# Optimization experiments

Measured on AMD Instinct MI355X. Metric: run time of the kernel, lower is better.

## Reference

```python
import jax, jax.numpy as jnp
import numpy as np

ALPHA = 0.6       # blend weight alpha
SEM_W = 0.5       # semantic_weight
PATCH = 3         # patch_size
EPS = 1e-5


def _mean_std(feat):
    # torch .var(dim=2) uses the unbiased estimator (ddof=1)
    N, C = feat.shape[:2]
    f = feat.reshape(N, C, -1)
    var = jnp.var(f, axis=2, ddof=1) + EPS
    return f.mean(axis=2).reshape(N, C, 1, 1), jnp.sqrt(var).reshape(N, C, 1, 1)


def _project(feat):
    m, s = _mean_std(feat)
    return (feat - m) / s


def _unfold(x, p):
    # torch x.unfold(2,p,1).unfold(3,p,1).permute(0,2,3,1,4,5).reshape(-1,C,p,p)
    N, C, H, W = x.shape
    Ho, Wo = H - p + 1, W - p + 1
    pats = jnp.stack([x[:, :, i:i + Ho, j:j + Wo]
                      for i in range(p) for j in range(p)], axis=-1)  # [N,C,Ho,Wo,p*p]
    return pats.transpose(0, 2, 3, 1, 4).reshape(N * Ho * Wo, C, p, p)


def _sgtw(sF, sF_fused, cF_fused, p):
    style_patches = _unfold(sF, p)        # [K, C, p, p]
    fused_patches = _unfold(sF_fused, p)  # [K, Cf, p, p]
    K = fused_patches.shape[0]
    norm = jnp.sqrt(jnp.sum(fused_patches.reshape(K, -1) ** 2, axis=1)).reshape(K, 1, 1, 1)
    kernels = fused_patches / (norm + 1e-7)
    # cross-correlation: content fused features vs normalized style patches
    coord = jax.lax.conv_general_dilated(
        cF_fused, kernels, (1, 1), 'VALID',
        dimension_numbers=('NCHW', 'OIHW', 'NCHW'))  # [N, K, Ho, Wo]
    idx = jnp.argmax(coord, axis=1)       # [N, Ho, Wo] hard top-1 patch match
    # one-hot scatter + conv_transpose2d == gather best patch + overlap-add
    sel = style_patches[idx]              # [N, Ho, Wo, C, p, p]
    N, Ho, Wo = idx.shape
    C = style_patches.shape[1]
    Hout, Wout = Ho + p - 1, Wo + p - 1
    out = jnp.zeros((N, C, Hout, Wout), sel.dtype)
    cnt = jnp.zeros((Hout, Wout), sel.dtype)
    for i in range(p):
        for j in range(p):
            out = out.at[:, :, i:i + Ho, j:j + Wo].add(sel[:, :, :, :, i, j].transpose(0, 3, 1, 2))
            cnt = cnt.at[i:i + Ho, j:j + Wo].add(1.0)
    return out / cnt[None, None]  # overlap-normalized reconstruction


def setup_inputs() -> dict:
    key = jax.random.key(0)
    k1, k2, k3, k4 = jax.random.split(key, 4)
    N, C, Cs, H, W = 1, 512, 64, 64, 64
    return {
        'cF': jax.random.normal(k1, (N, C, H, W), jnp.float32),
        'sF': jax.random.normal(k2, (N, C, H, W), jnp.float32),
        'cF_sem': jax.random.normal(k3, (N, Cs, H, W), jnp.float32),
        'sF_sem': jax.random.normal(k4, (N, Cs, H, W), jnp.float32),
    }


def reference(cF, sF, cF_sem, sF_sem):
    # VSTR_concat
    sF1 = _project(sF)
    cF1 = _project(cF)
    sF_fused = jnp.concatenate([sF1, SEM_W * sF_sem], axis=1)
    cF_fused = jnp.concatenate([cF1, SEM_W * cF_sem], axis=1)
    target = _sgtw(sF, sF_fused, cF_fused, PATCH).reshape(cF.shape)
    return ALPHA * target + (1.0 - ALPHA) * cF
```

## Files before the change

### kernel.cpp

```cpp
#include <hip/hip_runtime.h>
#include <hip/hip_bf16.h>

#define HW      4096
#define WIDTH   64
#define C_MAIN  512
#define C_F     576
#define HO      62
#define KPATCH  3844
#define ALPHA_W 0.6f
#define SEM_W   0.5f
#define EPS_V   1e-5f
#define DELTA   4e-3f

typedef __attribute__((ext_vector_type(8))) short bf16x8;
typedef __attribute__((ext_vector_type(4))) float f32x4;

__global__ __launch_bounds__(256) void stats_kernel(
    const float* __restrict__ cF, const float* __restrict__ sF,
    float4* __restrict__ stats) {
  int b = blockIdx.x;
  int tensor = b >> 9, c = b & 511;
  const float* src = (tensor ? sF : cF) + (size_t)c * HW;
  int t = threadIdx.x;
  float sum = 0.f, sumsq = 0.f;
#pragma unroll
  for (int i = 0; i < 4; ++i) {
    float4 v = *(const float4*)(src + (i * 256 + t) * 4);
    sum   += v.x + v.y + v.z + v.w;
    sumsq += v.x * v.x + v.y * v.y + v.z * v.z + v.w * v.w;
  }
#pragma unroll
  for (int off = 32; off; off >>= 1) {
    sum   += __shfl_down(sum, off, 64);
    sumsq += __shfl_down(sumsq, off, 64);
  }
  __shared__ float ls[8];
  int lane = t & 63, wv = t >> 6;
  if (lane == 0) { ls[wv] = sum; ls[4 + wv] = sumsq; }
  __syncthreads();
  if (t == 0) {
    float s  = ls[0] + ls[1] + ls[2] + ls[3];
    float sq = ls[4] + ls[5] + ls[6] + ls[7];
    float mean = s / 4096.f;
    float var  = (sq - 4096.f * mean * mean) / 4095.f;
    float sig  = sqrtf(var + EPS_V);
    stats[b] = make_float4(mean, 1.f / sig, sig, 0.f);
  }
}

__global__ __launch_bounds__(256) void transform_kernel(
    const float* __restrict__ cF, const float* __restrict__ sF,
    const float* __restrict__ cSem, const float* __restrict__ sSem,
    const float4* __restrict__ stats,
    unsigned short* __restrict__ Ahi, unsigned short* __restrict__ Alo,
    unsigned short* __restrict__ Bhi, unsigned short* __restrict__ Blo,
    float* __restrict__ sFfT) {
  int tensor = blockIdx.z;
  int p0 = blockIdx.x * 32, k0 = blockIdx.y * 32;
  __shared__ float tile[32][33];
  int tx = threadIdx.x & 31, ty = threadIdx.x >> 5;
  for (int r = ty; r < 32; r += 8) {
    int ch = k0 + r;
    float x;
    if (ch < C_MAIN) {
      const float* src = tensor ? sF : cF;
      float4 st = stats[tensor * 512 + ch];
      x = (src[(size_t)ch * HW + p0 + tx] - st.x) * st.y;
    } else {
      const float* src = tensor ? sSem : cSem;
      x = SEM_W * src[(size_t)(ch - C_MAIN) * HW + p0 + tx];
    }
    tile[r][tx] = x;
  }
  __syncthreads();
  unsigned short* dhi = tensor ? Bhi : Ahi;
  unsigned short* dlo = tensor ? Blo : Alo;
  for (int r = ty; r < 32; r += 8) {
    float x = tile[tx][r];
    __hip_bfloat16 hb = __float2bfloat16(x);
    float hf = __bfloat162float(hb);
    __hip_bfloat16 lb = __float2bfloat16(x - hf);
    size_t o = (size_t)(p0 + r) * C_F + k0 + tx;
    dhi[o] = *reinterpret_cast<const unsigned short*>(&hb);
    dlo[o] = *reinterpret_cast<const unsigned short*>(&lb);
    if (tensor) sFfT[o] = x;
  }
}

__global__ __launch_bounds__(256) void gemm_kernel(
    const unsigned short* __restrict__ Ahi, const unsigned short* __restrict__ Alo,
    const unsigned short* __restrict__ Bhi, const unsigned short* __restrict__ Blo,
    float* __restrict__ M) {
  __shared__ __align__(16) unsigned short As_hi[128 * 32];
  __shared__ __align__(16) unsigned short As_lo[128 * 32];
  __shared__ __align__(16) unsigned short Bs_hi[128 * 32];
  __shared__ __align__(16) unsigned short Bs_lo[128 * 32];
  int a0 = blockIdx.x * 128, u0 = blockIdx.y * 128;
  int t = threadIdx.x;
  int lane = t & 63, wave = t >> 6;
  int wr = wave >> 1, wc = wave & 1;
  int l15 = lane & 15, hig = lane >> 4;

  int sr = t >> 2;
  int sc = (t & 3) * 8;
  const unsigned short* Ag0 = Ahi + (size_t)(a0 + sr) * C_F + sc;
  const unsigned short* Ag1 = Alo + (size_t)(a0 + sr) * C_F + sc;
  const unsigned short* Bg0 = Bhi + (size_t)(u0 + sr) * C_F + sc;
  const unsigned short* Bg1 = Blo + (size_t)(u0 + sr) * C_F + sc;
  const size_t rstep = (size_t)64 * C_F;

  uint4 pah0 = *(const uint4*)(Ag0), pah1 = *(const uint4*)(Ag0 + rstep);
  uint4 pal0 = *(const uint4*)(Ag1), pal1 = *(const uint4*)(Ag1 + rstep);
  uint4 pbh0 = *(const uint4*)(Bg0), pbh1 = *(const uint4*)(Bg0 + rstep);
  uint4 pbl0 = *(const uint4*)(Bg1), pbl1 = *(const uint4*)(Bg1 + rstep);

  f32x4 zero4 = {0.f, 0.f, 0.f, 0.f};
  f32x4 acc[4][4];
#pragma unroll
  for (int m = 0; m < 4; ++m)
#pragma unroll
    for (int n = 0; n < 4; ++n) acc[m][n] = zero4;

  int lw = sr * 4 + (t & 3);
  for (int k0 = 0; k0 < C_F; k0 += 32) {
    __syncthreads();
    ((uint4*)As_hi)[lw] = pah0; ((uint4*)As_hi)[lw + 256] = pah1;
    ((uint4*)As_lo)[lw] = pal0; ((uint4*)As_lo)[lw + 256] = pal1;
    ((uint4*)Bs_hi)[lw] = pbh0; ((uint4*)Bs_hi)[lw + 256] = pbh1;
    ((uint4*)Bs_lo)[lw] = pbl0; ((uint4*)Bs_lo)[lw + 256] = pbl1;
    __syncthreads();
    if (k0 + 32 < C_F) {
      Ag0 += 32; Ag1 += 32; Bg0 += 32; Bg1 += 32;
      pah0 = *(const uint4*)(Ag0); pah1 = *(const uint4*)(Ag0 + rstep);
      pal0 = *(const uint4*)(Ag1); pal1 = *(const uint4*)(Ag1 + rstep);
      pbh0 = *(const uint4*)(Bg0); pbh1 = *(const uint4*)(Bg0 + rstep);
      pbl0 = *(const uint4*)(Bg1); pbl1 = *(const uint4*)(Bg1 + rstep);
    }
    bf16x8 bh[4], bl[4];
#pragma unroll
    for (int n = 0; n < 4; ++n) {
      int brow = wc * 64 + n * 16 + l15;
      bh[n] = *(const bf16x8*)&Bs_hi[brow * 32 + hig * 8];
      bl[n] = *(const bf16x8*)&Bs_lo[brow * 32 + hig * 8];
    }
#pragma unroll
    for (int m = 0; m < 4; ++m) {
      int arow = wr * 64 + m * 16 + l15;
      bf16x8 ah = *(const bf16x8*)&As_hi[arow * 32 + hig * 8];
      bf16x8 al = *(const bf16x8*)&As_lo[arow * 32 + hig * 8];
#pragma unroll
      for (int n = 0; n < 4; ++n) {
        acc[m][n] = __builtin_amdgcn_mfma_f32_16x16x32_bf16(ah, bh[n], acc[m][n], 0, 0, 0);
        acc[m][n] = __builtin_amdgcn_mfma_f32_16x16x32_bf16(ah, bl[n], acc[m][n], 0, 0, 0);
        acc[m][n] = __builtin_amdgcn_mfma_f32_16x16x32_bf16(al, bh[n], acc[m][n], 0, 0, 0);
      }
    }
  }
#pragma unroll
  for (int m = 0; m < 4; ++m) {
    int row = a0 + wr * 64 + m * 16 + hig * 4;
#pragma unroll
    for (int n = 0; n < 4; ++n) {
      int col = u0 + wc * 64 + n * 16 + l15;
#pragma unroll
      for (int r = 0; r < 4; ++r)
        M[(size_t)(row + r) * HW + col] = acc[m][n][r];
    }
  }
}

__global__ __launch_bounds__(256) void colsumsq_kernel(
    const float* __restrict__ sFfT, float* __restrict__ q) {
  int row = blockIdx.x * 4 + (threadIdx.x >> 6);
  int lane = threadIdx.x & 63;
  const float* r = sFfT + (size_t)row * C_F;
  float s = 0.f;
  for (int i = lane; i < C_F; i += 64) { float v = r[i]; s += v * v; }
#pragma unroll
  for (int off = 32; off; off >>= 1) s += __shfl_down(s, off, 64);
  if (lane == 0) q[row] = s;
}

__global__ __launch_bounds__(256) void rnorm_kernel(
    const float* __restrict__ q, float* __restrict__ rnorm) {
  int k = blockIdx.x * 256 + threadIdx.x;
  if (k >= KPATCH) return;
  int ky = k / HO, kx = k - ky * HO;
  float s = 0.f;
#pragma unroll
  for (int i = 0; i < 3; ++i)
#pragma unroll
    for (int j = 0; j < 3; ++j) s += q[(ky + i) * WIDTH + kx + j];
  rnorm[k] = 1.f / (sqrtf(s) + 1e-7f);
}

__global__ __launch_bounds__(256) void argmax_kernel(
    const float* __restrict__ M, const float* __restrict__ rnorm,
    const float* __restrict__ sFfT,
    const float* __restrict__ cF, const float* __restrict__ cSem,
    const float4* __restrict__ stats,
    int* __restrict__ idx) {
  int y0 = blockIdx.x * 2;
  int x0 = min((int)blockIdx.y * 4, HO - 4);
  int t = threadIdx.x;

  const float* Mbase = M + (size_t)(y0 * WIDTH + x0) * HW;
  int ijo[9];
#pragma unroll
  for (int i = 0; i < 3; ++i)
#pragma unroll
    for (int j = 0; j < 3; ++j)
      ijo[i * 3 + j] = (i * WIDTH + j) * HW + i * WIDTH + j;

  float v1[8], v2[8];
  int   k1[8], k2[8];
#pragma unroll
  for (int p = 0; p < 8; ++p) { v1[p] = -1e30f; v2[p] = -1e30f; k1[p] = 0; k2[p] = 0; }

  for (int k = t; k < KPATCH; k += 256) {
    int ky = k / HO;
    int u = k + 2 * ky;
    float s[8];
#pragma unroll
    for (int p = 0; p < 8; ++p) s[p] = 0.f;
#pragma unroll
    for (int o = 0; o < 9; ++o) {
      const float* p9 = Mbase + ijo[o] + u;
#pragma unroll
      for (int py = 0; py < 2; ++py)
#pragma unroll
        for (int px = 0; px < 4; ++px)
          s[py * 4 + px] += p9[(size_t)(py * WIDTH + px) * HW];
    }
    float rn = rnorm[k];
#pragma unroll
    for (int p = 0; p < 8; ++p) {
      float v = s[p] * rn;
      if (v > v1[p]) { v2[p] = v1[p]; k2[p] = k1[p]; v1[p] = v; k1[p] = k; }
      else if (v > v2[p]) { v2[p] = v; k2[p] = k; }
    }
  }

  __shared__ float sv[256];
  __shared__ int   sk[256];
  __shared__ float redf[256];
  __shared__ float cpatch[9 * C_F];
  __shared__ int   candList[64];
  __shared__ int   candN;
  __shared__ float bestE;
  __shared__ int   bestK;

  for (int pp = 0; pp < 8; ++pp) {
    int py = pp >> 2, px = pp & 3;
    float mv1 = -1e30f, mv2 = -1e30f; int mk1 = 0;
#pragma unroll
    for (int q = 0; q < 8; ++q)
      if (q == pp) { mv1 = v1[q]; mv2 = v2[q]; mk1 = k1[q]; }

    __syncthreads();
    sv[t] = mv1; sk[t] = mk1;
    __syncthreads();
    for (int off = 128; off; off >>= 1) {
      if (t < off) {
        float ov = sv[t + off]; int ok = sk[t + off];
        if (ov > sv[t] || (ov == sv[t] && ok < sk[t])) { sv[t] = ov; sk[t] = ok; }
      }
      __syncthreads();
    }
    float vbest = sv[0];
    int   kbest = sk[0];
    float thr = vbest - DELTA;
    if (t == 0) candN = 0;
    __syncthreads();

    int poff = (py * WIDTH + px) * HW;
    if (mv2 >= thr) {
      for (int k = t; k < KPATCH; k += 256) {
        int ky = k / HO;
        int u = k + 2 * ky;
        float s = 0.f;
#pragma unroll
        for (int o = 0; o < 9; ++o) s += Mbase[(size_t)(poff + ijo[o]) + u];
        float v = s * rnorm[k];
        if (v >= thr && k != kbest) {
          int sl = atomicAdd(&candN, 1);
          if (sl < 64) candList[sl] = k;
        }
      }
    } else if (mv1 >= thr && mk1 != kbest) {
      int sl = atomicAdd(&candN, 1);
      if (sl < 64) candList[sl] = mk1;
    }
    __syncthreads();
    int nc = min(candN, 64);
    if (nc == 0) {
      if (t == 0) idx[(y0 + py) * HO + x0 + px] = kbest;
      continue;
    }

    int y = y0 + py, x = x0 + px;
    for (int f = t; f < 9 * C_F; f += 256) {
      int ij = f / C_F, c = f - ij * C_F;
      int pp2 = (y + ij / 3) * WIDTH + x + ij % 3;
      float cv;
      if (c < C_MAIN) {
        float4 st = stats[c];
        cv = (cF[(size_t)c * HW + pp2] - st.x) * st.y;
      } else {
        cv = SEM_W * cSem[(size_t)(c - C_MAIN) * HW + pp2];
      }
      cpatch[f] = cv;
    }
    __syncthreads();
    if (t == 0) { bestE = -1e30f; bestK = 0x7fffffff; }
    __syncthreads();

    for (int ci = -1; ci < nc; ++ci) {
      int k = (ci < 0) ? kbest : candList[ci];
      int ky = k / HO, kx = k - ky * HO;
      float part = 0.f;
      for (int f = t; f < 9 * C_F; f += 256) {
        int ij = f / C_F, c = f - ij * C_F;
        int sp = (ky + ij / 3) * WIDTH + kx + ij % 3;
        part += cpatch[f] * sFfT[(size_t)sp * C_F + c];
      }
      redf[t] = part;
      __syncthreads();
      for (int off = 128; off; off >>= 1) {
        if (t < off) redf[t] += redf[t + off];
        __syncthreads();
      }
      if (t == 0) {
        float e = redf[0] * rnorm[k];
        if (e > bestE || (e == bestE && k < bestK)) { bestE = e; bestK = k; }
      }
      __syncthreads();
    }
    if (t == 0) idx[(y0 + py) * HO + x0 + px] = bestK;
  }
}

__global__ __launch_bounds__(256) void gather_kernel(
    const float* __restrict__ sFfT, const int* __restrict__ idx,
    float* __restrict__ tmp) {
  __shared__ int srcs[9];
  __shared__ int nv;
  int pix = blockIdx.x;
  int h = pix >> 6, w = pix & 63;
  if (threadIdx.x == 0) {
    int n = 0;
    for (int i = 0; i < 3; ++i)
      for (int j = 0; j < 3; ++j) {
        int y = h - i, x = w - j;
        if (y >= 0 && y < HO && x >= 0 && x < HO) {
          int k = idx[y * HO + x];
          int ky = k / HO, kx = k - ky * HO;
          srcs[n++] = (ky + i) * WIDTH + kx + j;
        }
      }
    nv = n;
  }
  __syncthreads();
  int n = nv;
  for (int c = threadIdx.x; c < C_MAIN; c += 256) {
    float acc = 0.f;
    for (int s = 0; s < n; ++s) acc += sFfT[(size_t)srcs[s] * C_F + c];
    tmp[(size_t)pix * C_MAIN + c] = acc;
  }
}

__global__ void blend_kernel(
    const float* __restrict__ tmp, const float* __restrict__ cF,
    const float4* __restrict__ stats, float* __restrict__ out) {
  __shared__ float tile[32][33];
  int p0 = blockIdx.x * 32;
  int c0 = blockIdx.y * 32;
  int tx = threadIdx.x, ty = threadIdx.y;
  for (int r = ty; r < 32; r += 8)
    tile[r][tx] = tmp[(size_t)(p0 + r) * C_MAIN + c0 + tx];
  __syncthreads();
  for (int r = ty; r < 32; r += 8) {
    int pix = p0 + tx;
    int h = pix >> 6, w = pix & 63;
    int nh = min(2, h) - max(0, h - 61) + 1;
    int nw = min(2, w) - max(0, w - 61) + 1;
    float inv_cnt = 1.f / (float)(nh * nw);
    int c = c0 + r;
    float4 st = stats[512 + c];
    float recon = st.z * (tile[tx][r] * inv_cnt) + st.x;
    out[(size_t)c * HW + pix] =
        ALPHA_W * recon + (1.f - ALPHA_W) * cF[(size_t)c * HW + pix];
  }
}

extern "C" void kernel_launch(void* const* d_in, const int* in_sizes, int n_in,
                              void* d_out, int out_size, void* d_ws, size_t ws_size,
                              hipStream_t stream) {
  const float* cF   = (const float*)d_in[0];
  const float* sF   = (const float*)d_in[1];
  const float* cSem = (const float*)d_in[2];
  const float* sSem = (const float*)d_in[3];
  float* out = (float*)d_out;

  char* ws = (char*)d_ws;
  unsigned short* Ahi = (unsigned short*)ws;
  unsigned short* Alo = Ahi + (size_t)HW * C_F;
  unsigned short* Bhi = Alo + (size_t)HW * C_F;
  unsigned short* Blo = Bhi + (size_t)HW * C_F;
  float* tmp  = (float*)ws;
  float* M    = (float*)(ws + 18874368);
  float* sFfT = (float*)(ws + 85983232);
  float* q    = (float*)(ws + 95420416);
  float* rnrm = (float*)(ws + 95420416 + 16384);
  int*   idx  = (int*)  (ws + 95420416 + 32768);
  float4* stats = (float4*)(ws + 95420416 + 49152);

  stats_kernel<<<1024, 256, 0, stream>>>(cF, sF, stats);
  transform_kernel<<<dim3(HW / 32, C_F / 32, 2), 256, 0, stream>>>(
      cF, sF, cSem, sSem, stats, Ahi, Alo, Bhi, Blo, sFfT);
  colsumsq_kernel<<<HW / 4, 256, 0, stream>>>(sFfT, q);
  rnorm_kernel<<<(KPATCH + 255) / 256, 256, 0, stream>>>(q, rnrm);
  gemm_kernel<<<dim3(32, 32), 256, 0, stream>>>(Ahi, Alo, Bhi, Blo, M);
  argmax_kernel<<<dim3(31, 16), 256, 0, stream>>>(M, rnrm, sFfT, cF, cSem, stats, idx);
  gather_kernel<<<HW, 256, 0, stream>>>(sFfT, idx, tmp);
  blend_kernel<<<dim3(128, 16), dim3(32, 8), 0, stream>>>(tmp, cF, stats, out);
}
```

Baseline: 225.0 us.

## Split argmax over patch chunks into partial top-2 kernel plus merge kernel

The argmax pass over the 3844 style patches moves into a separate kernel that splits the patch range into 4 chunks along a new grid dimension. Each block writes a per-position top-2 (value, index) partial result. A merge kernel combines the partials, builds the near-tie candidate list from them, and rescans only the chunks whose second-best clears the threshold before doing the exact refinement. The aim is to raise parallelism from 496 blocks to 1984 on a large GPU. The cost is an extra launch, a partial-results buffer in the workspace, and a tree reduction that now carries top-2 pairs.

```diff
diff --git a/kernel.cpp b/kernel.cpp
--- a/kernel.cpp
+++ b/kernel.cpp
@@ -11,6 +11,8 @@
 #define SEM_W   0.5f
 #define EPS_V   1e-5f
 #define DELTA   4e-3f
+#define NCHUNK  4
+#define CHUNKK  961
 
 typedef __attribute__((ext_vector_type(8))) short bf16x8;
 typedef __attribute__((ext_vector_type(4))) float f32x4;
@@ -194,8 +196,92 @@
   rnorm[k] = 1.f / (sqrtf(s) + 1e-7f);
 }
 
-__global__ __launch_bounds__(256) void argmax_kernel(
+__global__ __launch_bounds__(256) void argmax_part_kernel(
     const float* __restrict__ M, const float* __restrict__ rnorm,
+    float4* __restrict__ part) {
+  int y0 = blockIdx.x * 2;
+  int x0 = min((int)blockIdx.y * 4, HO - 4);
+  int cz = blockIdx.z;
+  int t = threadIdx.x;
+  int kbeg = cz * CHUNKK, kend = kbeg + CHUNKK;
+
+  const float* Mbase = M + (size_t)(y0 * WIDTH + x0) * HW;
+  int ijo[9];
+#pragma unroll
+  for (int i = 0; i < 3; ++i)
+#pragma unroll
+    for (int j = 0; j < 3; ++j)
+      ijo[i * 3 + j] = (i * WIDTH + j) * HW + i * WIDTH + j;
+
+  float v1[8], v2[8];
+  int   k1[8], k2[8];
+#pragma unroll
+  for (int p = 0; p < 8; ++p) { v1[p] = -1e30f; v2[p] = -1e30f; k1[p] = 0; k2[p] = 0; }
+
+  for (int k = kbeg + t; k < kend; k += 256) {
+    int ky = k / HO;
+    int u = k + 2 * ky;
+    float s[8];
+#pragma unroll
+    for (int p = 0; p < 8; ++p) s[p] = 0.f;
+#pragma unroll
+    for (int o = 0; o < 9; ++o) {
+      const float* p9 = Mbase + ijo[o] + u;
+#pragma unroll
+      for (int py = 0; py < 2; ++py)
+#pragma unroll
+        for (int px = 0; px < 4; ++px)
+          s[py * 4 + px] += p9[(size_t)(py * WIDTH + px) * HW];
+    }
+    float rn = rnorm[k];
+#pragma unroll
+    for (int p = 0; p < 8; ++p) {
+      float v = s[p] * rn;
+      if (v > v1[p]) { v2[p] = v1[p]; k2[p] = k1[p]; v1[p] = v; k1[p] = k; }
+      else if (v > v2[p]) { v2[p] = v; k2[p] = k; }
+    }
+  }
+
+  __shared__ float s1[256], s2[256];
+  __shared__ int   i1[256], i2[256];
+  for (int pp = 0; pp < 8; ++pp) {
+    float mv1 = -1e30f, mv2 = -1e30f; int mk1 = 0, mk2 = 0;
+#pragma unroll
+    for (int q = 0; q < 8; ++q)
+      if (q == pp) { mv1 = v1[q]; mv2 = v2[q]; mk1 = k1[q]; mk2 = k2[q]; }
+    __syncthreads();
+    s1[t] = mv1; i1[t] = mk1; s2[t] = mv2; i2[t] = mk2;
+    __syncthreads();
+    for (int off = 128; off; off >>= 1) {
+      if (t < off) {
+        float a1 = s1[t], a2 = s2[t];       int ka1 = i1[t],       ka2 = i2[t];
+        float b1 = s1[t + off], b2 = s2[t + off]; int kb1 = i1[t + off], kb2 = i2[t + off];
+        float n1, n2; int nk1, nk2;
+        if (b1 > a1 || (b1 == a1 && kb1 < ka1)) {
+          n1 = b1; nk1 = kb1;
+          if (a1 > b2 || (a1 == b2 && ka1 < kb2)) { n2 = a1; nk2 = ka1; }
+          else                                    { n2 = b2; nk2 = kb2; }
+        } else {
+          n1 = a1; nk1 = ka1;
+          if (b1 > a2 || (b1 == a2 && kb1 < ka2)) { n2 = b1; nk2 = kb1; }
+          else                                    { n2 = a2; nk2 = ka2; }
+        }
+        s1[t] = n1; i1[t] = nk1; s2[t] = n2; i2[t] = nk2;
+      }
+      __syncthreads();
+    }
+    if (t == 0) {
+      int py = pp >> 2, px = pp & 3;
+      int pos = (y0 + py) * HO + x0 + px;
+      part[pos * NCHUNK + cz] =
+          make_float4(s1[0], __int_as_float(i1[0]), s2[0], __int_as_float(i2[0]));
+    }
+  }
+}
+
+__global__ __launch_bounds__(256) void argmax_merge_kernel(
+    const float* __restrict__ M, const float* __restrict__ rnorm,
+    const float4* __restrict__ part,
     const float* __restrict__ sFfT,
     const float* __restrict__ cF, const float* __restrict__ cSem,
     const float4* __restrict__ stats,
@@ -212,37 +298,6 @@
     for (int j = 0; j < 3; ++j)
       ijo[i * 3 + j] = (i * WIDTH + j) * HW + i * WIDTH + j;
 
-  float v1[8], v2[8];
-  int   k1[8], k2[8];
-#pragma unroll
-  for (int p = 0; p < 8; ++p) { v1[p] = -1e30f; v2[p] = -1e30f; k1[p] = 0; k2[p] = 0; }
-
-  for (int k = t; k < KPATCH; k += 256) {
-    int ky = k / HO;
-    int u = k + 2 * ky;
-    float s[8];
-#pragma unroll
-    for (int p = 0; p < 8; ++p) s[p] = 0.f;
-#pragma unroll
-    for (int o = 0; o < 9; ++o) {
-      const float* p9 = Mbase + ijo[o] + u;
-#pragma unroll
-      for (int py = 0; py < 2; ++py)
-#pragma unroll
-        for (int px = 0; px < 4; ++px)
-          s[py * 4 + px] += p9[(size_t)(py * WIDTH + px) * HW];
-    }
-    float rn = rnorm[k];
-#pragma unroll
-    for (int p = 0; p < 8; ++p) {
-      float v = s[p] * rn;
-      if (v > v1[p]) { v2[p] = v1[p]; k2[p] = k1[p]; v1[p] = v; k1[p] = k; }
-      else if (v > v2[p]) { v2[p] = v; k2[p] = k; }
-    }
-  }
-
-  __shared__ float sv[256];
-  __shared__ int   sk[256];
   __shared__ float redf[256];
   __shared__ float cpatch[9 * C_F];
   __shared__ int   candList[64];
@@ -252,49 +307,59 @@
 
   for (int pp = 0; pp < 8; ++pp) {
     int py = pp >> 2, px = pp & 3;
-    float mv1 = -1e30f, mv2 = -1e30f; int mk1 = 0;
-#pragma unroll
-    for (int q = 0; q < 8; ++q)
-      if (q == pp) { mv1 = v1[q]; mv2 = v2[q]; mk1 = k1[q]; }
-
-    __syncthreads();
-    sv[t] = mv1; sk[t] = mk1;
-    __syncthreads();
-    for (int off = 128; off; off >>= 1) {
-      if (t < off) {
-        float ov = sv[t + off]; int ok = sk[t + off];
-        if (ov > sv[t] || (ov == sv[t] && ok < sk[t])) { sv[t] = ov; sk[t] = ok; }
-      }
-      __syncthreads();
-    }
-    float vbest = sv[0];
-    int   kbest = sk[0];
+    int pos = (y0 + py) * HO + x0 + px;
+
+    float cv1[NCHUNK], cv2[NCHUNK];
+    int   ck1[NCHUNK], ck2[NCHUNK];
+#pragma unroll
+    for (int c = 0; c < NCHUNK; ++c) {
+      float4 e = part[pos * NCHUNK + c];
+      cv1[c] = e.x; ck1[c] = __float_as_int(e.y);
+      cv2[c] = e.z; ck2[c] = __float_as_int(e.w);
+    }
+    float vbest = -1e30f; int kbest = 0x7fffffff;
+#pragma unroll
+    for (int c = 0; c < NCHUNK; ++c)
+      if (cv1[c] > vbest || (cv1[c] == vbest && ck1[c] < kbest)) {
+        vbest = cv1[c]; kbest = ck1[c];
+      }
     float thr = vbest - DELTA;
-    if (t == 0) candN = 0;
+
+    __syncthreads();
+    if (t == 0) {
+      int n = 0;
+#pragma unroll
+      for (int c = 0; c < NCHUNK; ++c) {
+        if (cv1[c] >= thr && ck1[c] != kbest && n < 64) candList[n++] = ck1[c];
+        if (cv2[c] >= thr && ck2[c] != kbest && n < 64) candList[n++] = ck2[c];
+      }
+      candN = n;
+    }
     __syncthreads();
 
     int poff = (py * WIDTH + px) * HW;
-    if (mv2 >= thr) {
-      for (int k = t; k < KPATCH; k += 256) {
-        int ky = k / HO;
-        int u = k + 2 * ky;
-        float s = 0.f;
-#pragma unroll
-        for (int o = 0; o < 9; ++o) s += Mbase[(size_t)(poff + ijo[o]) + u];
-        float v = s * rnorm[k];
-        if (v >= thr && k != kbest) {
-          int sl = atomicAdd(&candN, 1);
-          if (sl < 64) candList[sl] = k;
+#pragma unroll
+    for (int c = 0; c < NCHUNK; ++c) {
+      if (cv2[c] >= thr) {
+        for (int k = c * CHUNKK + t; k < (c + 1) * CHUNKK; k += 256) {
+          if (k == ck1[c] || k == ck2[c]) continue;
+          int ky = k / HO;
+          int u = k + 2 * ky;
+          float s = 0.f;
+#pragma unroll
+          for (int o = 0; o < 9; ++o) s += Mbase[(size_t)(poff + ijo[o]) + u];
+          float v = s * rnorm[k];
+          if (v >= thr) {
+            int sl = atomicAdd(&candN, 1);
+            if (sl < 64) candList[sl] = k;
+          }
         }
       }
-    } else if (mv1 >= thr && mk1 != kbest) {
-      int sl = atomicAdd(&candN, 1);
-      if (sl < 64) candList[sl] = mk1;
     }
     __syncthreads();
     int nc = min(candN, 64);
     if (nc == 0) {
-      if (t == 0) idx[(y0 + py) * HO + x0 + px] = kbest;
+      if (t == 0) idx[pos] = kbest;
       continue;
     }
 
@@ -318,13 +383,13 @@
     for (int ci = -1; ci < nc; ++ci) {
       int k = (ci < 0) ? kbest : candList[ci];
       int ky = k / HO, kx = k - ky * HO;
-      float part = 0.f;
+      float partsum = 0.f;
       for (int f = t; f < 9 * C_F; f += 256) {
         int ij = f / C_F, c = f - ij * C_F;
         int sp = (ky + ij / 3) * WIDTH + kx + ij % 3;
-        part += cpatch[f] * sFfT[(size_t)sp * C_F + c];
-      }
-      redf[t] = part;
+        partsum += cpatch[f] * sFfT[(size_t)sp * C_F + c];
+      }
+      redf[t] = partsum;
       __syncthreads();
       for (int off = 128; off; off >>= 1) {
         if (t < off) redf[t] += redf[t + off];
@@ -336,7 +401,7 @@
       }
       __syncthreads();
     }
-    if (t == 0) idx[(y0 + py) * HO + x0 + px] = bestK;
+    if (t == 0) idx[pos] = bestK;
   }
 }
 
@@ -414,6 +479,7 @@
   float* rnrm = (float*)(ws + 95420416 + 16384);
   int*   idx  = (int*)  (ws + 95420416 + 32768);
   float4* stats = (float4*)(ws + 95420416 + 49152);
+  float4* part  = (float4*)(ws + 95485952);
 
   stats_kernel<<<1024, 256, 0, stream>>>(cF, sF, stats);
   transform_kernel<<<dim3(HW / 32, C_F / 32, 2), 256, 0, stream>>>(
@@ -421,7 +487,9 @@
   colsumsq_kernel<<<HW / 4, 256, 0, stream>>>(sFfT, q);
   rnorm_kernel<<<(KPATCH + 255) / 256, 256, 0, stream>>>(q, rnrm);
   gemm_kernel<<<dim3(32, 32), 256, 0, stream>>>(Ahi, Alo, Bhi, Blo, M);
-  argmax_kernel<<<dim3(31, 16), 256, 0, stream>>>(M, rnrm, sFfT, cF, cSem, stats, idx);
+  argmax_part_kernel<<<dim3(31, 16, NCHUNK), 256, 0, stream>>>(M, rnrm, part);
+  argmax_merge_kernel<<<dim3(31, 16), 256, 0, stream>>>(
+      M, rnrm, part, sFfT, cF, cSem, stats, idx);
   gather_kernel<<<HW, 256, 0, stream>>>(sFfT, idx, tmp);
   blend_kernel<<<dim3(128, 16), dim3(32, 8), 0, stream>>>(tmp, cF, stats, out);
 }
```

New measurement: 273.4 us. 1.22x slower.
